# Performance work log

Hardware: AMD Instinct MI355X
Metric: run time of the kernel (lower is better)

Reference implementation:

```python
import jax, jax.numpy as jnp
import numpy as np

B, N, D, H, S = 2, 1024, 1024, 16, 4
DH = D // H  # dim_head = 64


def setup_inputs() -> dict:
    key = jax.random.key(0)
    ks = jax.random.split(key, 7)
    w = lambda k, shape: jax.random.normal(k, shape, dtype=jnp.float32) * 0.02
    return {
        "x": jax.random.normal(ks[0], (B, N, D), dtype=jnp.float32),
        "Wq": w(ks[1], (S, D, D)),
        "Wk": w(ks[2], (S, D, D)),
        "Wv": w(ks[3], (S, D, D)),
        "Wg": w(ks[4], (S, D)),
        "bg": jnp.zeros((S,), jnp.float32),
        "Wo": w(ks[5], (D, D)),
        "bo": jnp.zeros((D,), jnp.float32),
        "hyp_w": jnp.ones((S,), jnp.float32),
        "temperature": jnp.float32(1.0),
    }


def reference(x, Wq, Wk, Wv, Wg, bg, Wo, bo, hyp_w, temperature):
    # Training branch of EnhancedUncertaintyAttention, all S samples batched.
    b, n, d = x.shape
    scale = DH ** -0.5
    temp = jnp.clip(temperature, 0.1, 10.0)

    # coherence gate on mean-pooled tokens: [b, S]
    coh = jax.nn.sigmoid(x.mean(axis=1) @ Wg.T + bg)

    def proj(W):  # torch Linear: x @ W.T ; W: [S, out, in] -> [s,b,h,n,dh]
        y = jnp.einsum('bnd,sed->sbne', x, W)
        return y.reshape(S, b, n, H, DH).transpose(0, 1, 3, 2, 4)

    q, k, v = proj(Wq), proj(Wk), proj(Wv)

    dots = jnp.einsum('sbhid,sbhjd->sbhij', q, k) * scale
    attn = jax.nn.softmax(dots / temp, axis=-1)            # [S,b,h,n,n]
    out = jnp.einsum('sbhij,sbhjd->sbhid', attn, v)        # [S,b,h,n,dh]
    out = out.transpose(0, 1, 3, 2, 4).reshape(S, b, n, d) # [S,b,n,d]
    out = out * coh.T[:, :, None, None]                    # per-sample gate

    gw = jax.nn.softmax(hyp_w / temp)                      # hypothesis weights [S]
    combined = jnp.einsum('s,sbnd->bnd', gw, out)
    combined_attn = jnp.einsum('s,sbhij->bhij', gw, attn)

    y = combined @ Wo.T + bo  # to_out; dropout p treated as 0 (deterministic)
    return y, combined_attn.mean(axis=1)
```

## Files before the change

kernel.cpp:

```cpp
#include <hip/hip_runtime.h>
#include <hip/hip_bf16.h>

typedef __attribute__((ext_vector_type(8))) short s16x8;
typedef __attribute__((ext_vector_type(4))) float f32x4;

#define MAT2M 2097152
#define PPAD 72

__device__ __forceinline__ unsigned short f2bf(float f) {
  union { float f; unsigned u; } c; c.f = f;
  unsigned u = c.u;
  unsigned r = (u + 0x7fffu + ((u >> 16) & 1u)) >> 16;
  return (unsigned short)r;
}

__device__ __forceinline__ unsigned pk2bf(float a, float b) {
  union { __hip_bfloat162 h; unsigned u; } c;
  c.h = __float22bfloat162_rn(make_float2(a, b));
  return c.u;
}

__device__ __forceinline__ float bf2f(unsigned short u) {
  union { unsigned u; float f; } c; c.u = ((unsigned)u) << 16; return c.f;
}

__device__ __forceinline__ void async16(const unsigned short* g, unsigned short* l) {
  __builtin_amdgcn_global_load_lds(
      (const __attribute__((address_space(1))) unsigned int*)g,
      (__attribute__((address_space(3))) unsigned int*)l, 16, 0, 0);
}

__device__ __forceinline__ void stage64sw(const unsigned short* __restrict__ g,
                                          unsigned short* l, int wid, int ln) {
  const int rr = ln >> 3;
  const int gcol = ((ln & 7) ^ (rr & 7)) * 8;
#pragma unroll
  for (int c = 0; c < 2; ++c) {
    int r = (c * 4 + wid) * 8 + rr;
    async16(&g[(size_t)r * 1024 + gcol], &l[(c * 4 + wid) * 512 + ln * 8]);
  }
}

__global__ __launch_bounds__(256) void k_cvt(const float* __restrict__ in,
                                             unsigned short* __restrict__ out, int n) {
  int i = (blockIdx.x * 256 + threadIdx.x) * 4;
  if (i < n) {
    float4 v = *(const float4*)&in[i];
    ushort4 o;
    o.x = f2bf(v.x); o.y = f2bf(v.y); o.z = f2bf(v.z); o.w = f2bf(v.w);
    *(ushort4*)&out[i] = o;
  }
}

__global__ __launch_bounds__(256) void k_cvt3(const float* __restrict__ a,
                                              const float* __restrict__ b,
                                              const float* __restrict__ c,
                                              unsigned short* __restrict__ oa,
                                              unsigned short* __restrict__ ob,
                                              unsigned short* __restrict__ oc) {
  const float* in = blockIdx.y == 0 ? a : (blockIdx.y == 1 ? b : c);
  unsigned short* out = blockIdx.y == 0 ? oa : (blockIdx.y == 1 ? ob : oc);
  int i = (blockIdx.x * 256 + threadIdx.x) * 4;
  float4 v = *(const float4*)&in[i];
  ushort4 o;
  o.x = f2bf(v.x); o.y = f2bf(v.y); o.z = f2bf(v.z); o.w = f2bf(v.w);
  *(ushort4*)&out[i] = o;
}

__global__ __launch_bounds__(256) void k_meanx(const float* __restrict__ x,
                                               float* __restrict__ meanx) {
  int col = blockIdx.x * 256 + threadIdx.x;
  int b = col >> 10, d = col & 1023;
  int n0 = blockIdx.y * 64;
  float s = 0.f;
  for (int n = 0; n < 64; ++n)
    s += x[(size_t)b * 1048576 + (size_t)(n0 + n) * 1024 + d];
  atomicAdd(&meanx[col], s * (1.f / 1024.f));
}

__global__ __launch_bounds__(256) void k_prep(const float* __restrict__ meanx,
                                              const float* __restrict__ Wg,
                                              const float* __restrict__ bg,
                                              const float* __restrict__ hyp,
                                              const float* __restrict__ temp_p,
                                              float* __restrict__ prep) {
  int tid = threadIdx.x;
  int p = tid >> 5, c = tid & 31;
  int s = p >> 1, b = p & 1;
  float partial = 0.f;
  for (int d = c; d < 1024; d += 32)
    partial += meanx[b * 1024 + d] * Wg[s * 1024 + d];
#pragma unroll
  for (int m = 16; m >= 1; m >>= 1) partial += __shfl_xor(partial, m, 64);
  if (c == 0) {
    float coh = 1.f / (1.f + __expf(-(partial + bg[s])));
    prep[4 + s * 2 + b] = coh;
  }
  if (tid == 0) {
    float t = temp_p[0];
    t = fminf(fmaxf(t, 0.1f), 10.f);
    float it = 1.f / t;
    float e0 = hyp[0] * it, e1 = hyp[1] * it, e2 = hyp[2] * it, e3 = hyp[3] * it;
    float mx = fmaxf(fmaxf(e0, e1), fmaxf(e2, e3));
    float x0 = __expf(e0 - mx), x1 = __expf(e1 - mx), x2 = __expf(e2 - mx), x3 = __expf(e3 - mx);
    float inv = 1.f / (x0 + x1 + x2 + x3);
    prep[0] = x0 * inv; prep[1] = x1 * inv; prep[2] = x2 * inv; prep[3] = x3 * inv;
    prep[12] = 0.125f * it * 1.44269504f;
  }
}

__global__ __launch_bounds__(256) void gemm_qkv(
    const unsigned short* __restrict__ xb,
    const unsigned short* __restrict__ wqb,
    const unsigned short* __restrict__ wkb,
    const unsigned short* __restrict__ wvb,
    const float* __restrict__ prep,
    unsigned short* __restrict__ qk,
    unsigned short* __restrict__ vt) {
  __shared__ __align__(16) unsigned short As[128 * 64];
  __shared__ __align__(16) unsigned short Bs[128 * 64];
  const int tid = threadIdx.x;
  const int wid = tid >> 6, ln = tid & 63, lq = ln >> 4, lc = ln & 15;
  const int wr = wid >> 1, wc = wid & 1;
  const int z = blockIdx.z, proj = z >> 2, s = z & 3;
  const unsigned short* Bmat =
      (proj == 0 ? wqb : (proj == 1 ? wkb : wvb)) + (size_t)s * 1048576;
  const int n0 = blockIdx.x * 128, m0 = blockIdx.y * 128;
  const int sr = wid * 8 + (ln >> 3);
  const int sc = (((ln & 7) ^ ((ln >> 3) & 7))) * 8;
  const int ldsoff = wid * 512 + ln * 8;

  f32x4 acc[4][4];
#pragma unroll
  for (int a = 0; a < 4; ++a)
#pragma unroll
    for (int b4 = 0; b4 < 4; ++b4) acc[a][b4] = (f32x4){0.f, 0.f, 0.f, 0.f};

  for (int kt = 0; kt < 16; ++kt) {
    const int k0 = kt * 64;
    __syncthreads();
#pragma unroll
    for (int c = 0; c < 4; ++c) {
      async16(&xb[(size_t)(m0 + c * 32 + sr) * 1024 + k0 + sc], &As[c * 2048 + ldsoff]);
      async16(&Bmat[(size_t)(n0 + c * 32 + sr) * 1024 + k0 + sc], &Bs[c * 2048 + ldsoff]);
    }
    __syncthreads();
#pragma unroll
    for (int kc = 0; kc < 2; ++kc) {
      const int slot = ((kc * 4 + lq) ^ (lc & 7)) * 8;
      s16x8 af[4], bf[4];
#pragma unroll
      for (int a = 0; a < 4; ++a)
        af[a] = *(const s16x8*)&As[(wr * 64 + a * 16 + lc) * 64 + slot];
#pragma unroll
      for (int b4 = 0; b4 < 4; ++b4)
        bf[b4] = *(const s16x8*)&Bs[(wc * 64 + b4 * 16 + lc) * 64 + slot];
#pragma unroll
      for (int a = 0; a < 4; ++a)
#pragma unroll
        for (int b4 = 0; b4 < 4; ++b4)
          acc[a][b4] = __builtin_amdgcn_mfma_f32_16x16x32_bf16(af[a], bf[b4], acc[a][b4], 0, 0, 0);
    }
  }

  const float mulv = (proj == 1) ? prep[12] : 1.0f;
  if (z < 8) {
    unsigned short* C = qk + (size_t)z * MAT2M;
#pragma unroll
    for (int a = 0; a < 4; ++a) {
      int row0 = m0 + wr * 64 + a * 16 + lq * 4;
#pragma unroll
      for (int b4 = 0; b4 < 4; ++b4) {
        int col = n0 + wc * 64 + b4 * 16 + lc;
#pragma unroll
        for (int r = 0; r < 4; ++r)
          C[(size_t)(row0 + r) * 1024 + col] = f2bf(acc[a][b4][r] * mulv);
      }
    }
  } else {
#pragma unroll
    for (int a = 0; a < 4; ++a) {
      int row0 = m0 + wr * 64 + a * 16 + lq * 4;
      int bb = row0 >> 10, ii = row0 & 1023;
#pragma unroll
      for (int b4 = 0; b4 < 4; ++b4) {
        int col = n0 + wc * 64 + b4 * 16 + lc;
        int head = col >> 6, dh = col & 63;
        uint2 pk;
        pk.x = pk2bf(acc[a][b4][0], acc[a][b4][1]);
        pk.y = pk2bf(acc[a][b4][2], acc[a][b4][3]);
        *(uint2*)&vt[(((size_t)((s * 2 + bb) * 16 + head)) << 16) + dh * 1024 + ii] = pk;
      }
    }
  }
}

__global__ __launch_bounds__(256) void att_o(
    const unsigned short* __restrict__ qk,
    const unsigned short* __restrict__ vt,
    unsigned short* __restrict__ o_sb,
    float* __restrict__ linv_ws) {
  __shared__ __align__(16) unsigned short Ks[64 * 64];
  __shared__ __align__(16) unsigned short Vs[64 * 64];
  __shared__ __align__(16) unsigned short PB[8 * 16 * PPAD];

  const int tid = threadIdx.x;
  const int wid = tid >> 6, ln = tid & 63, lq = ln >> 4, lc = ln & 15;
  const int i0 = blockIdx.x * 128;
  const int h = blockIdx.y;
  const int sb = blockIdx.z, s = sb >> 1, b = sb & 1;

  const unsigned short* Qg =
      qk + (size_t)s * MAT2M + (size_t)(b * 1024 + i0 + wid * 32) * 1024 + h * 64;
  const unsigned short* Kg = qk + (size_t)(4 + s) * MAT2M + (size_t)b * 1048576 + h * 64;
  const unsigned short* Vtg = vt + (((size_t)(sb * 16 + h)) << 16);

  s16x8 qf[2][2];
#pragma unroll
  for (int g = 0; g < 2; ++g)
#pragma unroll
    for (int kc = 0; kc < 2; ++kc)
      qf[g][kc] = *(const s16x8*)&Qg[(size_t)(g * 16 + lc) * 1024 + kc * 32 + lq * 8];

  f32x4 oaccT[2][4];
#pragma unroll
  for (int g = 0; g < 2; ++g)
#pragma unroll
    for (int db = 0; db < 4; ++db) oaccT[g][db] = (f32x4){0.f, 0.f, 0.f, 0.f};
  float lsum[2] = {0.f, 0.f};
  unsigned short* PBw = PB + wid * 2 * 16 * PPAD;

  for (int jt = 0; jt < 16; ++jt) {
    __syncthreads();
    stage64sw(Kg + (size_t)jt * 64 * 1024, Ks, wid, ln);
    stage64sw(Vtg + jt * 64, Vs, wid, ln);
    __syncthreads();

    f32x4 st[2][4];
#pragma unroll
    for (int g = 0; g < 2; ++g)
#pragma unroll
      for (int jb = 0; jb < 4; ++jb) st[g][jb] = (f32x4){0.f, 0.f, 0.f, 0.f};
#pragma unroll
    for (int kc = 0; kc < 2; ++kc) {
      const int slot = ((kc * 4 + lq) ^ (lc & 7)) * 8;
#pragma unroll
      for (int jb = 0; jb < 4; ++jb) {
        s16x8 kf = *(const s16x8*)&Ks[(jb * 16 + lc) * 64 + slot];
        st[0][jb] = __builtin_amdgcn_mfma_f32_16x16x32_bf16(kf, qf[0][kc], st[0][jb], 0, 0, 0);
        st[1][jb] = __builtin_amdgcn_mfma_f32_16x16x32_bf16(kf, qf[1][kc], st[1][jb], 0, 0, 0);
      }
    }

#pragma unroll
    for (int g = 0; g < 2; ++g)
#pragma unroll
      for (int jb = 0; jb < 4; ++jb) {
        float p0 = __builtin_amdgcn_exp2f(st[g][jb][0]);
        float p1 = __builtin_amdgcn_exp2f(st[g][jb][1]);
        float p2 = __builtin_amdgcn_exp2f(st[g][jb][2]);
        float p3 = __builtin_amdgcn_exp2f(st[g][jb][3]);
        lsum[g] += (p0 + p1) + (p2 + p3);
        uint2 pv;
        pv.x = pk2bf(p0, p1);
        pv.y = pk2bf(p2, p3);
        *(uint2*)&PBw[(g * 16 + lc) * PPAD + jb * 16 + lq * 4] = pv;
      }

#pragma unroll
    for (int kc = 0; kc < 2; ++kc) {
      const int slot = ((kc * 4 + lq) ^ (lc & 7)) * 8;
      s16x8 pf0 = *(const s16x8*)&PBw[lc * PPAD + kc * 32 + lq * 8];
      s16x8 pf1 = *(const s16x8*)&PBw[(16 + lc) * PPAD + kc * 32 + lq * 8];
#pragma unroll
      for (int db = 0; db < 4; ++db) {
        s16x8 vf = *(const s16x8*)&Vs[(db * 16 + lc) * 64 + slot];
        oaccT[0][db] = __builtin_amdgcn_mfma_f32_16x16x32_bf16(vf, pf0, oaccT[0][db], 0, 0, 0);
        oaccT[1][db] = __builtin_amdgcn_mfma_f32_16x16x32_bf16(vf, pf1, oaccT[1][db], 0, 0, 0);
      }
    }
  }

  float invl[2];
#pragma unroll
  for (int g = 0; g < 2; ++g) {
    lsum[g] += __shfl_xor(lsum[g], 16, 64);
    lsum[g] += __shfl_xor(lsum[g], 32, 64);
    invl[g] = 1.f / lsum[g];
  }
  if (lq == 0) {
    int base = (sb * 16 + h) * 1024 + i0 + wid * 32 + lc;
    linv_ws[base] = invl[0];
    linv_ws[base + 16] = invl[1];
  }

#pragma unroll
  for (int g = 0; g < 2; ++g) {
    int i = i0 + wid * 32 + g * 16 + lc;
    unsigned short* orow =
        o_sb + (size_t)s * MAT2M + (size_t)(b * 1024 + i) * 1024 + h * 64;
#pragma unroll
    for (int db = 0; db < 4; ++db) {
      f32x4 o = oaccT[g][db] * invl[g];
      uint2 pv;
      pv.x = pk2bf(o[0], o[1]);
      pv.y = pk2bf(o[2], o[3]);
      *(uint2*)&orow[db * 16 + lq * 4] = pv;
    }
  }
}

__global__ __launch_bounds__(256) void att_p(
    const unsigned short* __restrict__ qk,
    const float* __restrict__ prep,
    const float* __restrict__ linv_ws,
    float* __restrict__ out1) {
  __shared__ __align__(16) unsigned short Qs[128 * 64];
  __shared__ __align__(16) unsigned short Ks[64 * 64];
  const int tid = threadIdx.x;
  const int wid = tid >> 6, ln = tid & 63, lq = ln >> 4, lc = ln & 15;
  const int j0 = blockIdx.x * 64;
  const int i0 = blockIdx.y * 128;
  const int z = blockIdx.z, s = z >> 1, b = z & 1;
  const float wgt = prep[s] * (1.f / 16.f);

  const unsigned short* Qb = qk + (size_t)s * MAT2M + (size_t)(b * 1024 + i0) * 1024;
  const unsigned short* Kb = qk + (size_t)(4 + s) * MAT2M + (size_t)(b * 1024 + j0) * 1024;

  const int rr = ln >> 3;
  const int gcol = ((ln & 7) ^ (rr & 7)) * 8;

  f32x4 psum[2][4];
#pragma unroll
  for (int g = 0; g < 2; ++g)
#pragma unroll
    for (int jb = 0; jb < 4; ++jb) psum[g][jb] = (f32x4){0.f, 0.f, 0.f, 0.f};

  for (int h = 0; h < 16; ++h) {
    const int hoff = h * 64;
    __syncthreads();
#pragma unroll
    for (int c = 0; c < 4; ++c) {
      int r = (c * 4 + wid) * 8 + rr;
      async16(&Qb[(size_t)r * 1024 + hoff + gcol], &Qs[(c * 4 + wid) * 512 + ln * 8]);
    }
    stage64sw(Kb + hoff, Ks, wid, ln);
    __syncthreads();

    s16x8 qf[2][2];
#pragma unroll
    for (int kc = 0; kc < 2; ++kc) {
      const int slot = ((kc * 4 + lq) ^ (lc & 7)) * 8;
#pragma unroll
      for (int g = 0; g < 2; ++g)
        qf[g][kc] = *(const s16x8*)&Qs[(wid * 32 + g * 16 + lc) * 64 + slot];
    }
    float ilr[2];
#pragma unroll
    for (int g = 0; g < 2; ++g)
      ilr[g] = wgt * linv_ws[(z * 16 + h) * 1024 + i0 + wid * 32 + g * 16 + lc];

    f32x4 st[2][4];
#pragma unroll
    for (int g = 0; g < 2; ++g)
#pragma unroll
      for (int jb = 0; jb < 4; ++jb) st[g][jb] = (f32x4){0.f, 0.f, 0.f, 0.f};
#pragma unroll
    for (int kc = 0; kc < 2; ++kc) {
      const int slot = ((kc * 4 + lq) ^ (lc & 7)) * 8;
#pragma unroll
      for (int jb = 0; jb < 4; ++jb) {
        s16x8 kf = *(const s16x8*)&Ks[(jb * 16 + lc) * 64 + slot];
        st[0][jb] = __builtin_amdgcn_mfma_f32_16x16x32_bf16(kf, qf[0][kc], st[0][jb], 0, 0, 0);
        st[1][jb] = __builtin_amdgcn_mfma_f32_16x16x32_bf16(kf, qf[1][kc], st[1][jb], 0, 0, 0);
      }
    }
#pragma unroll
    for (int g = 0; g < 2; ++g)
#pragma unroll
      for (int jb = 0; jb < 4; ++jb)
#pragma unroll
        for (int r = 0; r < 4; ++r)
          psum[g][jb][r] += __builtin_amdgcn_exp2f(st[g][jb][r]) * ilr[g];
  }

#pragma unroll
  for (int g = 0; g < 2; ++g) {
    int i = i0 + wid * 32 + g * 16 + lc;
    float* row = out1 + (size_t)b * 1048576 + (size_t)i * 1024;
#pragma unroll
    for (int jb = 0; jb < 4; ++jb)
#pragma unroll
      for (int r = 0; r < 4; ++r)
        atomicAdd(&row[j0 + jb * 16 + lq * 4 + r], psum[g][jb][r]);
  }
}

__global__ __launch_bounds__(256) void k_combine(const unsigned short* __restrict__ o_sb,
                                                 const float* __restrict__ prep,
                                                 unsigned short* __restrict__ comb) {
  size_t base = (size_t)(blockIdx.x * 256 + threadIdx.x) * 4;
  int m = (int)(base >> 10);
  int b = m >> 10;
  float w0 = prep[0] * prep[4 + 0 * 2 + b];
  float w1 = prep[1] * prep[4 + 1 * 2 + b];
  float w2 = prep[2] * prep[4 + 2 * 2 + b];
  float w3 = prep[3] * prep[4 + 3 * 2 + b];
  ushort4 v0 = *(const ushort4*)&o_sb[base];
  ushort4 v1 = *(const ushort4*)&o_sb[(size_t)MAT2M + base];
  ushort4 v2 = *(const ushort4*)&o_sb[(size_t)2 * MAT2M + base];
  ushort4 v3 = *(const ushort4*)&o_sb[(size_t)3 * MAT2M + base];
  float ax = w0 * bf2f(v0.x) + w1 * bf2f(v1.x) + w2 * bf2f(v2.x) + w3 * bf2f(v3.x);
  float ay = w0 * bf2f(v0.y) + w1 * bf2f(v1.y) + w2 * bf2f(v2.y) + w3 * bf2f(v3.y);
  float az = w0 * bf2f(v0.z) + w1 * bf2f(v1.z) + w2 * bf2f(v2.z) + w3 * bf2f(v3.z);
  float aw = w0 * bf2f(v0.w) + w1 * bf2f(v1.w) + w2 * bf2f(v2.w) + w3 * bf2f(v3.w);
  uint2 o;
  o.x = pk2bf(ax, ay);
  o.y = pk2bf(az, aw);
  *(uint2*)&comb[base] = o;
}

__global__ __launch_bounds__(256) void gemm_out(
    const unsigned short* __restrict__ Amat,
    const unsigned short* __restrict__ Bmat,
    const float* __restrict__ bias,
    float* __restrict__ y) {
  __shared__ __align__(16) unsigned short As[128 * 64];
  __shared__ __align__(16) unsigned short Bs[128 * 64];
  const int tid = threadIdx.x;
  const int wid = tid >> 6, ln = tid & 63, lq = ln >> 4, lc = ln & 15;
  const int wr = wid >> 1, wc = wid & 1;
  const int n0 = blockIdx.x * 128, m0 = blockIdx.y * 128;
  const int sr = wid * 8 + (ln >> 3);
  const int sc = (((ln & 7) ^ ((ln >> 3) & 7))) * 8;
  const int ldsoff = wid * 512 + ln * 8;

  f32x4 acc[4][4];
#pragma unroll
  for (int a = 0; a < 4; ++a)
#pragma unroll
    for (int b4 = 0; b4 < 4; ++b4) acc[a][b4] = (f32x4){0.f, 0.f, 0.f, 0.f};

  for (int kt = 0; kt < 16; ++kt) {
    const int k0 = kt * 64;
    __syncthreads();
#pragma unroll
    for (int c = 0; c < 4; ++c) {
      async16(&Amat[(size_t)(m0 + c * 32 + sr) * 1024 + k0 + sc], &As[c * 2048 + ldsoff]);
      async16(&Bmat[(size_t)(n0 + c * 32 + sr) * 1024 + k0 + sc], &Bs[c * 2048 + ldsoff]);
    }
    __syncthreads();
#pragma unroll
    for (int kc = 0; kc < 2; ++kc) {
      const int slot = ((kc * 4 + lq) ^ (lc & 7)) * 8;
      s16x8 af[4], bf[4];
#pragma unroll
      for (int a = 0; a < 4; ++a)
        af[a] = *(const s16x8*)&As[(wr * 64 + a * 16 + lc) * 64 + slot];
#pragma unroll
      for (int b4 = 0; b4 < 4; ++b4)
        bf[b4] = *(const s16x8*)&Bs[(wc * 64 + b4 * 16 + lc) * 64 + slot];
#pragma unroll
      for (int a = 0; a < 4; ++a)
#pragma unroll
        for (int b4 = 0; b4 < 4; ++b4)
          acc[a][b4] = __builtin_amdgcn_mfma_f32_16x16x32_bf16(af[a], bf[b4], acc[a][b4], 0, 0, 0);
    }
  }

#pragma unroll
  for (int a = 0; a < 4; ++a) {
    int row0 = m0 + wr * 64 + a * 16 + lq * 4;
#pragma unroll
    for (int b4 = 0; b4 < 4; ++b4) {
      int col = n0 + wc * 64 + b4 * 16 + lc;
      float bv = bias[col];
#pragma unroll
      for (int r = 0; r < 4; ++r)
        y[(size_t)(row0 + r) * 1024 + col] = acc[a][b4][r] + bv;
    }
  }
}

extern "C" void kernel_launch(void* const* d_in, const int* in_sizes, int n_in,
                              void* d_out, int out_size, void* d_ws, size_t ws_size,
                              hipStream_t stream) {
  const float* x    = (const float*)d_in[0];
  const float* Wq   = (const float*)d_in[1];
  const float* Wk   = (const float*)d_in[2];
  const float* Wv   = (const float*)d_in[3];
  const float* Wg   = (const float*)d_in[4];
  const float* bg   = (const float*)d_in[5];
  const float* Wo   = (const float*)d_in[6];
  const float* bo   = (const float*)d_in[7];
  const float* hyp  = (const float*)d_in[8];
  const float* temp = (const float*)d_in[9];

  float* y = (float*)d_out;
  float* out1 = y + MAT2M;

  char* w = (char*)d_ws;
  size_t off = 0;
  auto alloc = [&](size_t bytes) { void* p = w + off; off += (bytes + 255) & ~(size_t)255; return p; };
  unsigned short* xb   = (unsigned short*)alloc((size_t)MAT2M * 2);
  unsigned short* wqb  = (unsigned short*)alloc((size_t)4 * 1048576 * 2);
  unsigned short* wkb  = (unsigned short*)alloc((size_t)4 * 1048576 * 2);
  unsigned short* wvb  = (unsigned short*)alloc((size_t)4 * 1048576 * 2);
  unsigned short* wob  = (unsigned short*)alloc((size_t)1048576 * 2);
  unsigned short* qk   = (unsigned short*)alloc((size_t)8 * MAT2M * 2);
  unsigned short* vt   = (unsigned short*)alloc((size_t)4 * MAT2M * 2);
  unsigned short* o_sb = (unsigned short*)alloc((size_t)4 * MAT2M * 2);
  unsigned short* comb = (unsigned short*)alloc((size_t)MAT2M * 2);
  float* linv  = (float*)alloc((size_t)131072 * 4);
  float* meanx = (float*)alloc((size_t)2048 * 4);
  float* prep  = (float*)alloc((size_t)16 * 4);

  k_cvt<<<2048, 256, 0, stream>>>(x, xb, MAT2M);
  k_cvt3<<<dim3(4096, 3), 256, 0, stream>>>(Wq, Wk, Wv, wqb, wkb, wvb);
  k_cvt<<<1024, 256, 0, stream>>>(Wo, wob, 1048576);

  hipMemsetAsync(meanx, 0, 2048 * sizeof(float), stream);
  hipMemsetAsync(out1, 0, (size_t)MAT2M * sizeof(float), stream);
  k_meanx<<<dim3(8, 16), 256, 0, stream>>>(x, meanx);
  k_prep<<<1, 256, 0, stream>>>(meanx, Wg, bg, hyp, temp, prep);

  gemm_qkv<<<dim3(8, 16, 12), 256, 0, stream>>>(xb, wqb, wkb, wvb, prep, qk, vt);

  att_o<<<dim3(8, 16, 8), 256, 0, stream>>>(qk, vt, o_sb, linv);
  att_p<<<dim3(16, 8, 8), 256, 0, stream>>>(qk, prep, linv, out1);

  k_combine<<<2048, 256, 0, stream>>>(o_sb, prep, comb);
  gemm_out<<<dim3(8, 16, 1), 256, 0, stream>>>(comb, wob, bo, y);
}
```

Measured before the change: 409.2 us.

## Double-buffer K/V/Q tiles in attention kernels and replace atomics with partial reduce

Both att_o and att_p now use two LDS buffers. The next K/V (or Q/K) tile is staged while the current one is computed, which drops one barrier per iteration. att_p no longer does float atomicAdds into the averaged attention map. It writes per-(sample,batch) partial maps to a new 32 MB workspace, and a new k_reduce kernel sums the four samples into out1, which also removes the memset of out1. This trades atomic contention for extra global write and read traffic and doubles LDS use per block, which may lower occupancy.

```diff
diff --git a/kernel.cpp b/kernel.cpp
--- a/kernel.cpp
+++ b/kernel.cpp
@@ -200,8 +200,8 @@
     const unsigned short* __restrict__ vt,
     unsigned short* __restrict__ o_sb,
     float* __restrict__ linv_ws) {
-  __shared__ __align__(16) unsigned short Ks[64 * 64];
-  __shared__ __align__(16) unsigned short Vs[64 * 64];
+  __shared__ __align__(16) unsigned short Ks[2][64 * 64];
+  __shared__ __align__(16) unsigned short Vs[2][64 * 64];
   __shared__ __align__(16) unsigned short PB[8 * 16 * PPAD];
 
   const int tid = threadIdx.x;
@@ -230,11 +230,16 @@
   float lsum[2] = {0.f, 0.f};
   unsigned short* PBw = PB + wid * 2 * 16 * PPAD;
 
+  stage64sw(Kg, Ks[0], wid, ln);
+  stage64sw(Vtg, Vs[0], wid, ln);
+
   for (int jt = 0; jt < 16; ++jt) {
+    const int u = jt & 1;
     __syncthreads();
-    stage64sw(Kg + (size_t)jt * 64 * 1024, Ks, wid, ln);
-    stage64sw(Vtg + jt * 64, Vs, wid, ln);
-    __syncthreads();
+    if (jt < 15) {
+      stage64sw(Kg + (size_t)(jt + 1) * 64 * 1024, Ks[u ^ 1], wid, ln);
+      stage64sw(Vtg + (jt + 1) * 64, Vs[u ^ 1], wid, ln);
+    }
 
     f32x4 st[2][4];
 #pragma unroll
@@ -246,7 +251,7 @@
       const int slot = ((kc * 4 + lq) ^ (lc & 7)) * 8;
 #pragma unroll
       for (int jb = 0; jb < 4; ++jb) {
-        s16x8 kf = *(const s16x8*)&Ks[(jb * 16 + lc) * 64 + slot];
+        s16x8 kf = *(const s16x8*)&Ks[u][(jb * 16 + lc) * 64 + slot];
         st[0][jb] = __builtin_amdgcn_mfma_f32_16x16x32_bf16(kf, qf[0][kc], st[0][jb], 0, 0, 0);
         st[1][jb] = __builtin_amdgcn_mfma_f32_16x16x32_bf16(kf, qf[1][kc], st[1][jb], 0, 0, 0);
       }
@@ -274,7 +279,7 @@
       s16x8 pf1 = *(const s16x8*)&PBw[(16 + lc) * PPAD + kc * 32 + lq * 8];
 #pragma unroll
       for (int db = 0; db < 4; ++db) {
-        s16x8 vf = *(const s16x8*)&Vs[(db * 16 + lc) * 64 + slot];
+        s16x8 vf = *(const s16x8*)&Vs[u][(db * 16 + lc) * 64 + slot];
         oaccT[0][db] = __builtin_amdgcn_mfma_f32_16x16x32_bf16(vf, pf0, oaccT[0][db], 0, 0, 0);
         oaccT[1][db] = __builtin_amdgcn_mfma_f32_16x16x32_bf16(vf, pf1, oaccT[1][db], 0, 0, 0);
       }
@@ -314,9 +319,9 @@
     const unsigned short* __restrict__ qk,
     const float* __restrict__ prep,
     const float* __restrict__ linv_ws,
-    float* __restrict__ out1) {
-  __shared__ __align__(16) unsigned short Qs[128 * 64];
-  __shared__ __align__(16) unsigned short Ks[64 * 64];
+    float* __restrict__ pp) {
+  __shared__ __align__(16) unsigned short Qs[2][128 * 64];
+  __shared__ __align__(16) unsigned short Ks[2][64 * 64];
   const int tid = threadIdx.x;
   const int wid = tid >> 6, ln = tid & 63, lq = ln >> 4, lc = ln & 15;
   const int j0 = blockIdx.x * 64;
@@ -336,16 +341,25 @@
 #pragma unroll
     for (int jb = 0; jb < 4; ++jb) psum[g][jb] = (f32x4){0.f, 0.f, 0.f, 0.f};
 
+#pragma unroll
+  for (int c = 0; c < 4; ++c) {
+    int r = (c * 4 + wid) * 8 + rr;
+    async16(&Qb[(size_t)r * 1024 + gcol], &Qs[0][(c * 4 + wid) * 512 + ln * 8]);
+  }
+  stage64sw(Kb, Ks[0], wid, ln);
+
   for (int h = 0; h < 16; ++h) {
-    const int hoff = h * 64;
+    const int u = h & 1;
     __syncthreads();
-#pragma unroll
-    for (int c = 0; c < 4; ++c) {
-      int r = (c * 4 + wid) * 8 + rr;
-      async16(&Qb[(size_t)r * 1024 + hoff + gcol], &Qs[(c * 4 + wid) * 512 + ln * 8]);
-    }
-    stage64sw(Kb + hoff, Ks, wid, ln);
-    __syncthreads();
+    if (h < 15) {
+      const int hoff = (h + 1) * 64;
+#pragma unroll
+      for (int c = 0; c < 4; ++c) {
+        int r = (c * 4 + wid) * 8 + rr;
+        async16(&Qb[(size_t)r * 1024 + hoff + gcol], &Qs[u ^ 1][(c * 4 + wid) * 512 + ln * 8]);
+      }
+      stage64sw(Kb + hoff, Ks[u ^ 1], wid, ln);
+    }
 
     s16x8 qf[2][2];
 #pragma unroll
@@ -353,7 +367,7 @@
       const int slot = ((kc * 4 + lq) ^ (lc & 7)) * 8;
 #pragma unroll
       for (int g = 0; g < 2; ++g)
-        qf[g][kc] = *(const s16x8*)&Qs[(wid * 32 + g * 16 + lc) * 64 + slot];
+        qf[g][kc] = *(const s16x8*)&Qs[u][(wid * 32 + g * 16 + lc) * 64 + slot];
     }
     float ilr[2];
 #pragma unroll
@@ -370,7 +384,7 @@
       const int slot = ((kc * 4 + lq) ^ (lc & 7)) * 8;
 #pragma unroll
       for (int jb = 0; jb < 4; ++jb) {
-        s16x8 kf = *(const s16x8*)&Ks[(jb * 16 + lc) * 64 + slot];
+        s16x8 kf = *(const s16x8*)&Ks[u][(jb * 16 + lc) * 64 + slot];
         st[0][jb] = __builtin_amdgcn_mfma_f32_16x16x32_bf16(kf, qf[0][kc], st[0][jb], 0, 0, 0);
         st[1][jb] = __builtin_amdgcn_mfma_f32_16x16x32_bf16(kf, qf[1][kc], st[1][jb], 0, 0, 0);
       }
@@ -384,16 +398,32 @@
           psum[g][jb][r] += __builtin_amdgcn_exp2f(st[g][jb][r]) * ilr[g];
   }
 
+  float* prow = pp + (size_t)z * 1048576;
 #pragma unroll
   for (int g = 0; g < 2; ++g) {
     int i = i0 + wid * 32 + g * 16 + lc;
-    float* row = out1 + (size_t)b * 1048576 + (size_t)i * 1024;
 #pragma unroll
     for (int jb = 0; jb < 4; ++jb)
-#pragma unroll
-      for (int r = 0; r < 4; ++r)
-        atomicAdd(&row[j0 + jb * 16 + lq * 4 + r], psum[g][jb][r]);
-  }
+      *(f32x4*)&prow[(size_t)i * 1024 + j0 + jb * 16 + lq * 4] = psum[g][jb];
+  }
+}
+
+__global__ __launch_bounds__(256) void k_reduce(const float* __restrict__ pp,
+                                                float* __restrict__ out1) {
+  size_t idx = ((size_t)blockIdx.x * 256 + threadIdx.x) * 4;
+  int b = (int)(idx >> 20);
+  size_t rem = idx & 1048575u;
+  const float* base = pp + (size_t)b * 1048576 + rem;
+  float4 a0 = *(const float4*)&base[0];
+  float4 a1 = *(const float4*)&base[(size_t)2 * 1048576];
+  float4 a2 = *(const float4*)&base[(size_t)4 * 1048576];
+  float4 a3 = *(const float4*)&base[(size_t)6 * 1048576];
+  float4 o;
+  o.x = (a0.x + a1.x) + (a2.x + a3.x);
+  o.y = (a0.y + a1.y) + (a2.y + a3.y);
+  o.z = (a0.z + a1.z) + (a2.z + a3.z);
+  o.w = (a0.w + a1.w) + (a2.w + a3.w);
+  *(float4*)&out1[idx] = o;
 }
 
 __global__ __launch_bounds__(256) void k_combine(const unsigned short* __restrict__ o_sb,
@@ -511,6 +541,7 @@
   unsigned short* vt   = (unsigned short*)alloc((size_t)4 * MAT2M * 2);
   unsigned short* o_sb = (unsigned short*)alloc((size_t)4 * MAT2M * 2);
   unsigned short* comb = (unsigned short*)alloc((size_t)MAT2M * 2);
+  float* pp    = (float*)alloc((size_t)8 * 1048576 * 4);
   float* linv  = (float*)alloc((size_t)131072 * 4);
   float* meanx = (float*)alloc((size_t)2048 * 4);
   float* prep  = (float*)alloc((size_t)16 * 4);
@@ -520,14 +551,14 @@
   k_cvt<<<1024, 256, 0, stream>>>(Wo, wob, 1048576);
 
   hipMemsetAsync(meanx, 0, 2048 * sizeof(float), stream);
-  hipMemsetAsync(out1, 0, (size_t)MAT2M * sizeof(float), stream);
   k_meanx<<<dim3(8, 16), 256, 0, stream>>>(x, meanx);
   k_prep<<<1, 256, 0, stream>>>(meanx, Wg, bg, hyp, temp, prep);
 
   gemm_qkv<<<dim3(8, 16, 12), 256, 0, stream>>>(xb, wqb, wkb, wvb, prep, qk, vt);
 
   att_o<<<dim3(8, 16, 8), 256, 0, stream>>>(qk, vt, o_sb, linv);
-  att_p<<<dim3(16, 8, 8), 256, 0, stream>>>(qk, prep, linv, out1);
+  att_p<<<dim3(16, 8, 8), 256, 0, stream>>>(qk, prep, linv, pp);
+  k_reduce<<<2048, 256, 0, stream>>>(pp, out1);
 
   k_combine<<<2048, 256, 0, stream>>>(o_sb, prep, comb);
   gemm_out<<<dim3(8, 16, 1), 256, 0, stream>>>(comb, wob, bo, y);
```

Result: faster. 341.4 us (-16.6%).
